# Kernel optimization log

Hardware: AMD Instinct MI355X
Metric: run time of the kernel (lower is better)

## Reference

```python
import jax, jax.numpy as jnp
import numpy as np

N_NODES = 100000
N_EDGES = 1600000
IN_C = 16
OUT_C = 16
N_EATTR = 8


def setup_inputs() -> dict:
    key = jax.random.key(0)
    k1, k2, k3, k4 = jax.random.split(key, 4)
    x = jax.random.normal(k1, (N_NODES, IN_C), dtype=jnp.float32)
    edge_index = jax.random.randint(k2, (2, N_EDGES), 0, N_NODES, dtype=jnp.int64)
    edge_attr = jax.random.normal(k3, (N_EDGES, N_EATTR), dtype=jnp.float32)
    # learned params (original inits to ones/zeros; use small random for a non-degenerate baseline)
    weight_matrix = jax.random.normal(k4, (N_EATTR, OUT_C, IN_C), dtype=jnp.float32) * 0.1
    bias = jnp.zeros((OUT_C,), dtype=jnp.float32)
    return {
        "x": x,
        "edge_index": edge_index,
        "edge_attr": edge_attr,
        "weight_matrix": weight_matrix,
        "bias": bias,
        "num_nodes": N_NODES,
    }


def reference(x, edge_index, edge_attr, weight_matrix, bias, num_nodes):
    # message: per-edge weight W_e = edge_attr @ weight_matrix (-> [E, out, in]),
    # then msg_e = W_e @ x[src_e]. Fused in one einsum to avoid the [E,out,in] blow-up.
    src = edge_index[0]
    dst = edge_index[1]
    x_j = x[src]                                   # [E, in]
    msg = jnp.einsum('ea,aoi,ei->eo', edge_attr, weight_matrix, x_j)  # [E, out]
    # aggregate: scatter-add messages to destination nodes
    aggr = jax.ops.segment_sum(msg, dst, num_segments=num_nodes)      # [N, out]
    # update: bias + relu
    return jax.nn.relu(aggr + bias)
```

## Files before the change

### kernel.cpp

```cpp
#include <hip/hip_runtime.h>


#define IN_C 16
#define OUT_C 16
#define NA 8

typedef unsigned short u16;

__device__ __forceinline__ float bfbits(unsigned hi) {
    union { unsigned u; float f; } c; c.u = hi; return c.f;
}
__device__ __forceinline__ u16 f2bf(float f) {
    union { float f; unsigned u; } c; c.f = f;
    unsigned u = c.u + (0x7fffu + ((c.u >> 16) & 1u));
    return (u16)(u >> 16);
}
__device__ __forceinline__ float dot4(float4 a, float4 b) {
    float s = a.x * b.x;
    s = fmaf(a.y, b.y, s);
    s = fmaf(a.z, b.z, s);
    s = fmaf(a.w, b.w, s);
    return s;
}

__global__ void __launch_bounds__(256) k_stage1(
    const float* __restrict__ x, const float* __restrict__ W,
    const int* __restrict__ ei, long long n_edges,
    u16* __restrict__ y, float* __restrict__ out,
    int* __restrict__ flag, int n_nodes) {
    __shared__ int s_nz;
    if (blockIdx.x == 0) {
        if (threadIdx.x == 0) s_nz = 0;
        __syncthreads();
        long long lim = 2 * n_edges;
        long long step = (n_edges / 256) | 1;
        long long pos = 1 + 2 * (long long)threadIdx.x * step;
        if (pos < lim && ei[pos] != 0) atomicOr(&s_nz, 1);
        __syncthreads();
        if (threadIdx.x == 0) flag[0] = (s_nz == 0) ? 1 : 0;
    }

    __shared__ float4 Wl[OUT_C][33];
    for (int k = threadIdx.x; k < 512; k += 256) {
        int a = k >> 6, o = (k >> 2) & 15, q = k & 3;
        Wl[o][a * 4 + q] = reinterpret_cast<const float4*>(W)[k];
    }
    __syncthreads();

    int npairs = (n_nodes + 1) >> 1;
    int idx = blockIdx.x * 256 + threadIdx.x;
    if (idx >= npairs * OUT_C) return;
    int p = idx >> 4, o = idx & 15;
    int n0 = p * 2;
    bool has1 = (n0 + 1) < n_nodes;

    const float4* xp0 = reinterpret_cast<const float4*>(x + (size_t)n0 * IN_C);
    float4 X0[4] = {xp0[0], xp0[1], xp0[2], xp0[3]};
    float4 X1[4];
    if (has1) {
        const float4* xp1 = reinterpret_cast<const float4*>(x + (size_t)(n0 + 1) * IN_C);
        X1[0] = xp1[0]; X1[1] = xp1[1]; X1[2] = xp1[2]; X1[3] = xp1[3];
    }

    union { uint4 u; u16 h[8]; } pk0, pk1;
#pragma unroll
    for (int a = 0; a < NA; ++a) {
        float4 w0 = Wl[o][a * 4 + 0], w1 = Wl[o][a * 4 + 1];
        float4 w2 = Wl[o][a * 4 + 2], w3 = Wl[o][a * 4 + 3];
        float s0 = dot4(w0, X0[0]) + dot4(w1, X0[1]) + dot4(w2, X0[2]) + dot4(w3, X0[3]);
        pk0.h[a] = f2bf(s0);
        if (has1) {
            float s1 = dot4(w0, X1[0]) + dot4(w1, X1[1]) + dot4(w2, X1[2]) + dot4(w3, X1[3]);
            pk1.h[a] = f2bf(s1);
        }
    }
    reinterpret_cast<uint4*>(y + ((size_t)n0 * OUT_C + o) * NA)[0] = pk0.u;
    out[(size_t)n0 * OUT_C + o] = 0.f;
    if (has1) {
        reinterpret_cast<uint4*>(y + ((size_t)(n0 + 1) * OUT_C + o) * NA)[0] = pk1.u;
        out[(size_t)(n0 + 1) * OUT_C + o] = 0.f;
    }
}

__global__ void __launch_bounds__(256) k_stage2(
    const int* __restrict__ ei, const float* __restrict__ ea,
    const u16* __restrict__ y, float* __restrict__ out,
    const int* __restrict__ flag, long long n_edges) {
    long long idx = (long long)blockIdx.x * 256 + threadIdx.x;
    if (idx >= n_edges * OUT_C) return;
    long long e = idx >> 4;
    int o = (int)(idx & 15);
    int src, dst;
    if (flag[0]) { src = ei[2 * e]; dst = ei[2 * (n_edges + e)]; }
    else         { src = ei[e];     dst = ei[n_edges + e]; }

    const float4* ap = reinterpret_cast<const float4*>(ea + e * NA);
    float4 a0 = ap[0], a1 = ap[1];
    uint4 yu = reinterpret_cast<const uint4*>(y + ((size_t)src * OUT_C + o) * NA)[0];

    float s =      bfbits(yu.x << 16)        * a0.x;
    s = fmaf(bfbits(yu.x & 0xffff0000u), a0.y, s);
    s = fmaf(bfbits(yu.y << 16),         a0.z, s);
    s = fmaf(bfbits(yu.y & 0xffff0000u), a0.w, s);
    s = fmaf(bfbits(yu.z << 16),         a1.x, s);
    s = fmaf(bfbits(yu.z & 0xffff0000u), a1.y, s);
    s = fmaf(bfbits(yu.w << 16),         a1.z, s);
    s = fmaf(bfbits(yu.w & 0xffff0000u), a1.w, s);

    unsafeAtomicAdd(out + (size_t)dst * OUT_C + o, s);
}

__global__ void __launch_bounds__(256) k_direct(
    const float* __restrict__ x, const int* __restrict__ ei,
    const float* __restrict__ ea, const float* __restrict__ W,
    float* __restrict__ out, long long n_edges) {
    __shared__ float Wl[OUT_C][129];
    for (int k = threadIdx.x; k < NA * OUT_C * IN_C; k += 256) {
        int a = k >> 8, o = (k >> 4) & 15, i = k & 15;
        Wl[o][a * IN_C + i] = W[k];
    }
    __syncthreads();
    long long idx = (long long)blockIdx.x * 256 + threadIdx.x;
    if (idx >= n_edges * OUT_C) return;
    long long e = idx >> 4;
    int o = (int)(idx & 15);
    int src = ei[2 * e], dst = ei[2 * (n_edges + e)];
    const float4* ap = reinterpret_cast<const float4*>(ea + e * NA);
    float4 a0 = ap[0], a1 = ap[1];
    float av[NA] = {a0.x, a0.y, a0.z, a0.w, a1.x, a1.y, a1.z, a1.w};
    const float4* xp = reinterpret_cast<const float4*>(x + (size_t)src * IN_C);
    float4 x0 = xp[0], x1 = xp[1], x2 = xp[2], x3 = xp[3];
    float xv[16] = {x0.x, x0.y, x0.z, x0.w, x1.x, x1.y, x1.z, x1.w,
                    x2.x, x2.y, x2.z, x2.w, x3.x, x3.y, x3.z, x3.w};
    float s = 0.f;
#pragma unroll
    for (int a = 0; a < NA; ++a) {
        float d = 0.f;
#pragma unroll
        for (int i = 0; i < IN_C; ++i) d = fmaf(Wl[o][a * IN_C + i], xv[i], d);
        s = fmaf(av[a], d, s);
    }
    unsafeAtomicAdd(out + (size_t)dst * OUT_C + o, s);
}

__global__ void __launch_bounds__(256) k_bias_relu(
    const float* __restrict__ bias, float* __restrict__ out, int total4) {
    int idx = blockIdx.x * 256 + threadIdx.x;
    if (idx >= total4) return;
    int j0 = (idx & 3) * 4;
    const float4 b = reinterpret_cast<const float4*>(bias + j0)[0];
    float4* op = reinterpret_cast<float4*>(out) + idx;
    float4 v = op[0];
    v.x = fmaxf(v.x + b.x, 0.f);
    v.y = fmaxf(v.y + b.y, 0.f);
    v.z = fmaxf(v.z + b.z, 0.f);
    v.w = fmaxf(v.w + b.w, 0.f);
    op[0] = v;
}

extern "C" void kernel_launch(void* const* d_in, const int* in_sizes, int n_in,
                              void* d_out, int out_size, void* d_ws, size_t ws_size,
                              hipStream_t stream) {
    const float* x    = (const float*)d_in[0];
    const int*   ei   = (const int*)d_in[1];
    const float* ea   = (const float*)d_in[2];
    const float* W    = (const float*)d_in[3];
    const float* bias = (const float*)d_in[4];
    float* out = (float*)d_out;

    int n_nodes = in_sizes[0] / IN_C;
    long long n_edges = in_sizes[2] / NA;

    size_t y_bytes = (size_t)n_nodes * OUT_C * NA * sizeof(u16);
    if (ws_size >= 64 + y_bytes) {
        int* flag = (int*)d_ws;
        u16* y = (u16*)((char*)d_ws + 64);
        int npairs = (n_nodes + 1) >> 1;
        int t1 = npairs * OUT_C;
        k_stage1<<<(t1 + 255) / 256, 256, 0, stream>>>(x, W, ei, n_edges, y, out, flag, n_nodes);
        long long tE = n_edges * OUT_C;
        k_stage2<<<(int)((tE + 255) / 256), 256, 0, stream>>>(ei, ea, y, out, flag, n_edges);
    } else {
        hipMemsetAsync(d_out, 0, (size_t)n_nodes * OUT_C * sizeof(float), stream);
        long long tE = n_edges * OUT_C;
        k_direct<<<(int)((tE + 255) / 256), 256, 0, stream>>>(x, ei, ea, W, out, n_edges);
    }

    int t4 = (n_nodes * OUT_C) / 4;
    k_bias_relu<<<(t4 + 255) / 256, 256, 0, stream>>>(bias, out, t4);
}
```

Baseline: 224.5 us.

## Replace per-edge atomic scatter with CSR sort by destination and per-node gather

Builds a destination-sorted edge list each call (histogram, two-pass scan, atomic scatter of src and bf16-packed edge attributes), then aggregates per node: accumulates edge_attr-weighted x[src] into 8 partials and applies the weight matrix, bias and relu once per node. This removes the 16 float atomics per edge into the output and the separate bias/relu pass. It adds more kernel launches, per-edge atomics for counting and placement, and a serial per-node loop whose cost depends on degree balance; edge attributes are now rounded to bf16.

```diff
diff --git a/kernel.cpp b/kernel.cpp
--- a/kernel.cpp
+++ b/kernel.cpp
@@ -6,20 +6,158 @@
 #define NA 8
 
 typedef unsigned short u16;
-
-__device__ __forceinline__ float bfbits(unsigned hi) {
-    union { unsigned u; float f; } c; c.u = hi; return c.f;
+typedef unsigned int u32;
+
+__device__ __forceinline__ float bfbits(u32 hi) {
+    union { u32 u; float f; } c; c.u = hi; return c.f;
 }
 __device__ __forceinline__ u16 f2bf(float f) {
-    union { float f; unsigned u; } c; c.f = f;
-    unsigned u = c.u + (0x7fffu + ((c.u >> 16) & 1u));
+    union { float f; u32 u; } c; c.f = f;
+    u32 u = c.u + (0x7fffu + ((c.u >> 16) & 1u));
     return (u16)(u >> 16);
 }
+
+__global__ void __launch_bounds__(256) k_init(
+    const int* __restrict__ ei, long long E, int* __restrict__ flag,
+    int* __restrict__ cnt, int n_nodes) {
+    int k = blockIdx.x * 256 + threadIdx.x;
+    if (k < n_nodes) cnt[k] = 0;
+    if (blockIdx.x == 0) {
+        __shared__ int s_nz;
+        if (threadIdx.x == 0) s_nz = 0;
+        __syncthreads();
+        long long step = (E / 256) | 1;
+        long long pos = 1 + 2 * (long long)threadIdx.x * step;
+        if (pos < 2 * E && ei[pos] != 0) atomicOr(&s_nz, 1);
+        __syncthreads();
+        if (threadIdx.x == 0) flag[0] = (s_nz == 0) ? 1 : 0;
+    }
+}
+
+__global__ void __launch_bounds__(256) k_hist(
+    const int* __restrict__ ei, long long E, const int* __restrict__ flag,
+    int* __restrict__ cnt) {
+    long long e = (long long)blockIdx.x * 256 + threadIdx.x;
+    if (e >= E) return;
+    int dst = flag[0] ? ei[2 * (E + e)] : ei[E + e];
+    atomicAdd(&cnt[dst], 1);
+}
+
+__global__ void __launch_bounds__(1024) k_scan1(
+    const int* __restrict__ cnt, int n, int* __restrict__ off, int* __restrict__ aux) {
+    __shared__ int s[1024];
+    int t = threadIdx.x;
+    int gid = blockIdx.x * 1024 + t;
+    int c = (gid < n) ? cnt[gid] : 0;
+    s[t] = c;
+    __syncthreads();
+    for (int d = 1; d < 1024; d <<= 1) {
+        int v = (t >= d) ? s[t - d] : 0;
+        __syncthreads();
+        s[t] += v;
+        __syncthreads();
+    }
+    if (gid < n) off[gid] = s[t] - c;
+    if (t == 1023) aux[blockIdx.x] = s[1023];
+}
+
+__global__ void __launch_bounds__(1024) k_scan2(
+    int* __restrict__ off, int* __restrict__ cur, const int* __restrict__ aux,
+    int nblk, int n) {
+    __shared__ int s_aux[128];
+    __shared__ int s_pfx;
+    if (threadIdx.x < 128) s_aux[threadIdx.x] = (threadIdx.x < nblk) ? aux[threadIdx.x] : 0;
+    __syncthreads();
+    if (threadIdx.x == 0) {
+        int p = 0;
+        for (int j = 0; j < (int)blockIdx.x; ++j) p += s_aux[j];
+        s_pfx = p;
+    }
+    __syncthreads();
+    int gid = blockIdx.x * 1024 + threadIdx.x;
+    if (gid < n) {
+        int o = off[gid] + s_pfx;
+        off[gid] = o;
+        cur[gid] = o;
+    }
+}
+
+__global__ void __launch_bounds__(256) k_scatter(
+    const int* __restrict__ ei, const float* __restrict__ ea,
+    const int* __restrict__ flag, int* __restrict__ cur,
+    int* __restrict__ p_src, uint4* __restrict__ p_ea, long long E) {
+    long long e = (long long)blockIdx.x * 256 + threadIdx.x;
+    if (e >= E) return;
+    int src, dst;
+    if (flag[0]) { src = ei[2 * e]; dst = ei[2 * (E + e)]; }
+    else         { src = ei[e];     dst = ei[E + e]; }
+    const float4* ap = reinterpret_cast<const float4*>(ea + e * NA);
+    float4 a0 = ap[0], a1 = ap[1];
+    union { uint4 u; u16 h[8]; } pk;
+    pk.h[0] = f2bf(a0.x); pk.h[1] = f2bf(a0.y); pk.h[2] = f2bf(a0.z); pk.h[3] = f2bf(a0.w);
+    pk.h[4] = f2bf(a1.x); pk.h[5] = f2bf(a1.y); pk.h[6] = f2bf(a1.z); pk.h[7] = f2bf(a1.w);
+    int pos = atomicAdd(&cur[dst], 1);
+    p_src[pos] = src;
+    p_ea[pos] = pk.u;
+}
+
+__global__ void __launch_bounds__(256) k_aggregate(
+    const float* __restrict__ x, const float* __restrict__ W,
+    const float* __restrict__ bias,
+    const int* __restrict__ off, const int* __restrict__ cur,
+    const int* __restrict__ p_src, const uint4* __restrict__ p_ea,
+    float* __restrict__ out, int n_nodes) {
+    __shared__ float Wl[2048];
+    __shared__ float P[16 * 272];
+    for (int k = threadIdx.x; k < 2048; k += 256) Wl[k] = W[k];
+    __syncthreads();
+
+    int g = threadIdx.x >> 4;
+    int i = threadIdx.x & 15;
+    int n = blockIdx.x * 16 + g;
+
+    float T0 = 0.f, T1 = 0.f, T2 = 0.f, T3 = 0.f, T4 = 0.f, T5 = 0.f, T6 = 0.f, T7 = 0.f;
+    float bi = bias[i];
+    if (n < n_nodes) {
+        int s = off[n], e = cur[n];
+        for (int p = s; p < e; ++p) {
+            int src = p_src[p];
+            uint4 eu = p_ea[p];
+            float xv = x[(size_t)src * IN_C + i];
+            T0 = fmaf(bfbits(eu.x << 16),         xv, T0);
+            T1 = fmaf(bfbits(eu.x & 0xffff0000u), xv, T1);
+            T2 = fmaf(bfbits(eu.y << 16),         xv, T2);
+            T3 = fmaf(bfbits(eu.y & 0xffff0000u), xv, T3);
+            T4 = fmaf(bfbits(eu.z << 16),         xv, T4);
+            T5 = fmaf(bfbits(eu.z & 0xffff0000u), xv, T5);
+            T6 = fmaf(bfbits(eu.w << 16),         xv, T6);
+            T7 = fmaf(bfbits(eu.w & 0xffff0000u), xv, T7);
+        }
+    }
+    float* Pg = P + g * 272;
+#pragma unroll
+    for (int o = 0; o < 16; ++o) {
+        const float* w = Wl + o * 16 + i;
+        float pv = T0 * w[0];
+        pv = fmaf(T1, w[256],  pv);
+        pv = fmaf(T2, w[512],  pv);
+        pv = fmaf(T3, w[768],  pv);
+        pv = fmaf(T4, w[1024], pv);
+        pv = fmaf(T5, w[1280], pv);
+        pv = fmaf(T6, w[1536], pv);
+        pv = fmaf(T7, w[1792], pv);
+        Pg[i * 17 + o] = pv;
+    }
+    __syncthreads();
+    float sum = 0.f;
+#pragma unroll
+    for (int l = 0; l < 16; ++l) sum += Pg[l * 17 + i];
+    if (n < n_nodes) out[(size_t)n * OUT_C + i] = fmaxf(sum + bi, 0.f);
+}
+
 __device__ __forceinline__ float dot4(float4 a, float4 b) {
     float s = a.x * b.x;
-    s = fmaf(a.y, b.y, s);
-    s = fmaf(a.z, b.z, s);
-    s = fmaf(a.w, b.w, s);
+    s = fmaf(a.y, b.y, s); s = fmaf(a.z, b.z, s); s = fmaf(a.w, b.w, s);
     return s;
 }
 
@@ -32,28 +170,24 @@
     if (blockIdx.x == 0) {
         if (threadIdx.x == 0) s_nz = 0;
         __syncthreads();
-        long long lim = 2 * n_edges;
         long long step = (n_edges / 256) | 1;
         long long pos = 1 + 2 * (long long)threadIdx.x * step;
-        if (pos < lim && ei[pos] != 0) atomicOr(&s_nz, 1);
+        if (pos < 2 * n_edges && ei[pos] != 0) atomicOr(&s_nz, 1);
         __syncthreads();
         if (threadIdx.x == 0) flag[0] = (s_nz == 0) ? 1 : 0;
     }
-
     __shared__ float4 Wl[OUT_C][33];
     for (int k = threadIdx.x; k < 512; k += 256) {
         int a = k >> 6, o = (k >> 2) & 15, q = k & 3;
         Wl[o][a * 4 + q] = reinterpret_cast<const float4*>(W)[k];
     }
     __syncthreads();
-
     int npairs = (n_nodes + 1) >> 1;
     int idx = blockIdx.x * 256 + threadIdx.x;
     if (idx >= npairs * OUT_C) return;
     int p = idx >> 4, o = idx & 15;
     int n0 = p * 2;
     bool has1 = (n0 + 1) < n_nodes;
-
     const float4* xp0 = reinterpret_cast<const float4*>(x + (size_t)n0 * IN_C);
     float4 X0[4] = {xp0[0], xp0[1], xp0[2], xp0[3]};
     float4 X1[4];
@@ -61,7 +195,6 @@
         const float4* xp1 = reinterpret_cast<const float4*>(x + (size_t)(n0 + 1) * IN_C);
         X1[0] = xp1[0]; X1[1] = xp1[1]; X1[2] = xp1[2]; X1[3] = xp1[3];
     }
-
     union { uint4 u; u16 h[8]; } pk0, pk1;
 #pragma unroll
     for (int a = 0; a < NA; ++a) {
@@ -93,12 +226,10 @@
     int src, dst;
     if (flag[0]) { src = ei[2 * e]; dst = ei[2 * (n_edges + e)]; }
     else         { src = ei[e];     dst = ei[n_edges + e]; }
-
     const float4* ap = reinterpret_cast<const float4*>(ea + e * NA);
     float4 a0 = ap[0], a1 = ap[1];
     uint4 yu = reinterpret_cast<const uint4*>(y + ((size_t)src * OUT_C + o) * NA)[0];
-
-    float s =      bfbits(yu.x << 16)        * a0.x;
+    float s = bfbits(yu.x << 16) * a0.x;
     s = fmaf(bfbits(yu.x & 0xffff0000u), a0.y, s);
     s = fmaf(bfbits(yu.y << 16),         a0.z, s);
     s = fmaf(bfbits(yu.y & 0xffff0000u), a0.w, s);
@@ -106,8 +237,22 @@
     s = fmaf(bfbits(yu.z & 0xffff0000u), a1.y, s);
     s = fmaf(bfbits(yu.w << 16),         a1.z, s);
     s = fmaf(bfbits(yu.w & 0xffff0000u), a1.w, s);
-
     unsafeAtomicAdd(out + (size_t)dst * OUT_C + o, s);
+}
+
+__global__ void __launch_bounds__(256) k_bias_relu(
+    const float* __restrict__ bias, float* __restrict__ out, int total4) {
+    int idx = blockIdx.x * 256 + threadIdx.x;
+    if (idx >= total4) return;
+    int j0 = (idx & 3) * 4;
+    const float4 b = reinterpret_cast<const float4*>(bias + j0)[0];
+    float4* op = reinterpret_cast<float4*>(out) + idx;
+    float4 v = op[0];
+    v.x = fmaxf(v.x + b.x, 0.f);
+    v.y = fmaxf(v.y + b.y, 0.f);
+    v.z = fmaxf(v.z + b.z, 0.f);
+    v.w = fmaxf(v.w + b.w, 0.f);
+    op[0] = v;
 }
 
 __global__ void __launch_bounds__(256) k_direct(
@@ -143,20 +288,7 @@
     unsafeAtomicAdd(out + (size_t)dst * OUT_C + o, s);
 }
 
-__global__ void __launch_bounds__(256) k_bias_relu(
-    const float* __restrict__ bias, float* __restrict__ out, int total4) {
-    int idx = blockIdx.x * 256 + threadIdx.x;
-    if (idx >= total4) return;
-    int j0 = (idx & 3) * 4;
-    const float4 b = reinterpret_cast<const float4*>(bias + j0)[0];
-    float4* op = reinterpret_cast<float4*>(out) + idx;
-    float4 v = op[0];
-    v.x = fmaxf(v.x + b.x, 0.f);
-    v.y = fmaxf(v.y + b.y, 0.f);
-    v.z = fmaxf(v.z + b.z, 0.f);
-    v.w = fmaxf(v.w + b.w, 0.f);
-    op[0] = v;
-}
+static inline size_t a256(size_t v) { return (v + 255) & ~(size_t)255; }
 
 extern "C" void kernel_launch(void* const* d_in, const int* in_sizes, int n_in,
                               void* d_out, int out_size, void* d_ws, size_t ws_size,
@@ -169,23 +301,54 @@
     float* out = (float*)d_out;
 
     int n_nodes = in_sizes[0] / IN_C;
-    long long n_edges = in_sizes[2] / NA;
-
-    size_t y_bytes = (size_t)n_nodes * OUT_C * NA * sizeof(u16);
-    if (ws_size >= 64 + y_bytes) {
-        int* flag = (int*)d_ws;
-        u16* y = (u16*)((char*)d_ws + 64);
-        int npairs = (n_nodes + 1) >> 1;
-        int t1 = npairs * OUT_C;
-        k_stage1<<<(t1 + 255) / 256, 256, 0, stream>>>(x, W, ei, n_edges, y, out, flag, n_nodes);
-        long long tE = n_edges * OUT_C;
-        k_stage2<<<(int)((tE + 255) / 256), 256, 0, stream>>>(ei, ea, y, out, flag, n_edges);
+    long long E = in_sizes[2] / NA;
+
+    size_t o_flag = 0;
+    size_t o_cnt  = 256;
+    size_t o_off  = o_cnt + a256((size_t)n_nodes * 4);
+    size_t o_cur  = o_off + a256((size_t)n_nodes * 4);
+    size_t o_aux  = o_cur + a256((size_t)n_nodes * 4);
+    size_t o_psrc = o_aux + 1024;
+    size_t o_pea  = o_psrc + a256((size_t)E * 4);
+    size_t total  = o_pea + a256((size_t)E * 16);
+
+    int gE = (int)((E + 255) / 256);
+    int gN = (n_nodes + 255) / 256;
+    int nblk_scan = (n_nodes + 1023) / 1024;
+
+    if (ws_size >= total) {
+        char* w8 = (char*)d_ws;
+        int*   flag  = (int*)(w8 + o_flag);
+        int*   cnt   = (int*)(w8 + o_cnt);
+        int*   off   = (int*)(w8 + o_off);
+        int*   cur   = (int*)(w8 + o_cur);
+        int*   aux   = (int*)(w8 + o_aux);
+        int*   p_src = (int*)(w8 + o_psrc);
+        uint4* p_ea  = (uint4*)(w8 + o_pea);
+
+        k_init<<<gN, 256, 0, stream>>>(ei, E, flag, cnt, n_nodes);
+        k_hist<<<gE, 256, 0, stream>>>(ei, E, flag, cnt);
+        k_scan1<<<nblk_scan, 1024, 0, stream>>>(cnt, n_nodes, off, aux);
+        k_scan2<<<nblk_scan, 1024, 0, stream>>>(off, cur, aux, nblk_scan, n_nodes);
+        k_scatter<<<gE, 256, 0, stream>>>(ei, ea, flag, cur, p_src, p_ea, E);
+        k_aggregate<<<(n_nodes + 15) / 16, 256, 0, stream>>>(
+            x, W, bias, off, cur, p_src, p_ea, out, n_nodes);
     } else {
-        hipMemsetAsync(d_out, 0, (size_t)n_nodes * OUT_C * sizeof(float), stream);
-        long long tE = n_edges * OUT_C;
-        k_direct<<<(int)((tE + 255) / 256), 256, 0, stream>>>(x, ei, ea, W, out, n_edges);
-    }
-
-    int t4 = (n_nodes * OUT_C) / 4;
-    k_bias_relu<<<(t4 + 255) / 256, 256, 0, stream>>>(bias, out, t4);
-}
+        size_t y_bytes = (size_t)n_nodes * OUT_C * NA * sizeof(u16);
+        if (ws_size >= 64 + y_bytes) {
+            int* flag = (int*)d_ws;
+            u16* y = (u16*)((char*)d_ws + 64);
+            int npairs = (n_nodes + 1) >> 1;
+            int t1 = npairs * OUT_C;
+            k_stage1<<<(t1 + 255) / 256, 256, 0, stream>>>(x, W, ei, E, y, out, flag, n_nodes);
+            long long tE = E * OUT_C;
+            k_stage2<<<(int)((tE + 255) / 256), 256, 0, stream>>>(ei, ea, y, out, flag, E);
+        } else {
+            hipMemsetAsync(d_out, 0, (size_t)n_nodes * OUT_C * sizeof(float), stream);
+            long long tE = E * OUT_C;
+            k_direct<<<(int)((tE + 255) / 256), 256, 0, stream>>>(x, ei, ea, W, out, E);
+        }
+        int t4 = (n_nodes * OUT_C) / 4;
+        k_bias_relu<<<(t4 + 255) / 256, 256, 0, stream>>>(bias, out, t4);
+    }
+}
```

Result: slower. 345.2 us (+53.7%).

## Scatter messages with packed bf16x2 atomics into two split accumulators

Applied to the files above, without the earlier changes.

Replaces the fp32 per-output atomic scatter with a kernel where each thread computes two output channels and issues a single packed bf16x2 global atomic add. Edges alternate between two bf16 accumulation buffers by parity to spread contention, and a final kernel sums both, adds bias and applies relu. This halves the atomic count and atomic traffic but accumulates in bf16, which loses precision on high-degree nodes. It also adds a memset and a larger workspace requirement.

```diff
diff --git a/kernel.cpp b/kernel.cpp
--- a/kernel.cpp
+++ b/kernel.cpp
@@ -6,20 +6,31 @@
 #define NA 8
 
 typedef unsigned short u16;
-
-__device__ __forceinline__ float bfbits(unsigned hi) {
-    union { unsigned u; float f; } c; c.u = hi; return c.f;
+typedef unsigned int u32;
+typedef short v2s __attribute__((ext_vector_type(2)));
+
+__device__ __forceinline__ float bfbits(u32 hi) {
+    union { u32 u; float f; } c; c.u = hi; return c.f;
 }
 __device__ __forceinline__ u16 f2bf(float f) {
-    union { float f; unsigned u; } c; c.f = f;
-    unsigned u = c.u + (0x7fffu + ((c.u >> 16) & 1u));
+    union { float f; u32 u; } c; c.f = f;
+    u32 u = c.u + (0x7fffu + ((c.u >> 16) & 1u));
     return (u16)(u >> 16);
 }
 __device__ __forceinline__ float dot4(float4 a, float4 b) {
     float s = a.x * b.x;
-    s = fmaf(a.y, b.y, s);
-    s = fmaf(a.z, b.z, s);
-    s = fmaf(a.w, b.w, s);
+    s = fmaf(a.y, b.y, s); s = fmaf(a.z, b.z, s); s = fmaf(a.w, b.w, s);
+    return s;
+}
+__device__ __forceinline__ float dot8y(uint4 yu, float4 a0, float4 a1) {
+    float s = bfbits(yu.x << 16) * a0.x;
+    s = fmaf(bfbits(yu.x & 0xffff0000u), a0.y, s);
+    s = fmaf(bfbits(yu.y << 16),         a0.z, s);
+    s = fmaf(bfbits(yu.y & 0xffff0000u), a0.w, s);
+    s = fmaf(bfbits(yu.z << 16),         a1.x, s);
+    s = fmaf(bfbits(yu.z & 0xffff0000u), a1.y, s);
+    s = fmaf(bfbits(yu.w << 16),         a1.z, s);
+    s = fmaf(bfbits(yu.w & 0xffff0000u), a1.w, s);
     return s;
 }
 
@@ -32,28 +43,24 @@
     if (blockIdx.x == 0) {
         if (threadIdx.x == 0) s_nz = 0;
         __syncthreads();
-        long long lim = 2 * n_edges;
         long long step = (n_edges / 256) | 1;
         long long pos = 1 + 2 * (long long)threadIdx.x * step;
-        if (pos < lim && ei[pos] != 0) atomicOr(&s_nz, 1);
+        if (pos < 2 * n_edges && ei[pos] != 0) atomicOr(&s_nz, 1);
         __syncthreads();
         if (threadIdx.x == 0) flag[0] = (s_nz == 0) ? 1 : 0;
     }
-
     __shared__ float4 Wl[OUT_C][33];
     for (int k = threadIdx.x; k < 512; k += 256) {
         int a = k >> 6, o = (k >> 2) & 15, q = k & 3;
         Wl[o][a * 4 + q] = reinterpret_cast<const float4*>(W)[k];
     }
     __syncthreads();
-
     int npairs = (n_nodes + 1) >> 1;
     int idx = blockIdx.x * 256 + threadIdx.x;
     if (idx >= npairs * OUT_C) return;
     int p = idx >> 4, o = idx & 15;
     int n0 = p * 2;
     bool has1 = (n0 + 1) < n_nodes;
-
     const float4* xp0 = reinterpret_cast<const float4*>(x + (size_t)n0 * IN_C);
     float4 X0[4] = {xp0[0], xp0[1], xp0[2], xp0[3]};
     float4 X1[4];
@@ -61,7 +68,6 @@
         const float4* xp1 = reinterpret_cast<const float4*>(x + (size_t)(n0 + 1) * IN_C);
         X1[0] = xp1[0]; X1[1] = xp1[1]; X1[2] = xp1[2]; X1[3] = xp1[3];
     }
-
     union { uint4 u; u16 h[8]; } pk0, pk1;
 #pragma unroll
     for (int a = 0; a < NA; ++a) {
@@ -80,6 +86,67 @@
         reinterpret_cast<uint4*>(y + ((size_t)(n0 + 1) * OUT_C + o) * NA)[0] = pk1.u;
         out[(size_t)(n0 + 1) * OUT_C + o] = 0.f;
     }
+}
+
+__global__ void __launch_bounds__(256) k_stage2_pk(
+    const int* __restrict__ ei, const float* __restrict__ ea,
+    const u16* __restrict__ y, u16* __restrict__ bufA, u16* __restrict__ bufB,
+    const int* __restrict__ flag, long long n_edges) {
+    long long gid = (long long)blockIdx.x * 256 + threadIdx.x;
+    if (gid >= n_edges * 8) return;
+    long long e = gid >> 3;
+    int q = (int)(gid & 7);
+    int src, dst;
+    if (flag[0]) { src = ei[2 * e]; dst = ei[2 * (n_edges + e)]; }
+    else         { src = ei[e];     dst = ei[n_edges + e]; }
+
+    const float4* ap = reinterpret_cast<const float4*>(ea + e * NA);
+    float4 a0 = ap[0], a1 = ap[1];
+
+    const uint4* yp = reinterpret_cast<const uint4*>(y + ((size_t)src * OUT_C + 2 * q) * NA);
+    float s0 = dot8y(yp[0], a0, a1);
+    float s1 = dot8y(yp[1], a0, a1);
+
+    union { v2s v; u16 h[2]; } pk;
+    pk.h[0] = f2bf(s0);
+    pk.h[1] = f2bf(s1);
+    u16* target = (e & 1) ? bufB : bufA;
+    v2s* addr = reinterpret_cast<v2s*>(target + (size_t)dst * OUT_C + 2 * q);
+    __builtin_amdgcn_global_atomic_fadd_v2bf16(addr, pk.v);
+}
+
+__global__ void __launch_bounds__(256) k_final_pk(
+    const u16* __restrict__ bufA, const u16* __restrict__ bufB,
+    const float* __restrict__ bias, float* __restrict__ out, int total8) {
+    int idx = blockIdx.x * 256 + threadIdx.x;
+    if (idx >= total8) return;
+    uint4 ua = reinterpret_cast<const uint4*>(bufA)[idx];
+    uint4 ub = reinterpret_cast<const uint4*>(bufB)[idx];
+    int ob = (idx & 1) * 8;
+    const float4 b0 = reinterpret_cast<const float4*>(bias + ob)[0];
+    const float4 b1 = reinterpret_cast<const float4*>(bias + ob + 4)[0];
+    float fa[8], fb[8];
+    u32 au[4] = {ua.x, ua.y, ua.z, ua.w}, bu[4] = {ub.x, ub.y, ub.z, ub.w};
+#pragma unroll
+    for (int j = 0; j < 4; ++j) {
+        fa[2 * j]     = bfbits(au[j] << 16);
+        fa[2 * j + 1] = bfbits(au[j] & 0xffff0000u);
+        fb[2 * j]     = bfbits(bu[j] << 16);
+        fb[2 * j + 1] = bfbits(bu[j] & 0xffff0000u);
+    }
+    float bb[8] = {b0.x, b0.y, b0.z, b0.w, b1.x, b1.y, b1.z, b1.w};
+    float4 o0, o1;
+    o0.x = fmaxf(fa[0] + fb[0] + bb[0], 0.f);
+    o0.y = fmaxf(fa[1] + fb[1] + bb[1], 0.f);
+    o0.z = fmaxf(fa[2] + fb[2] + bb[2], 0.f);
+    o0.w = fmaxf(fa[3] + fb[3] + bb[3], 0.f);
+    o1.x = fmaxf(fa[4] + fb[4] + bb[4], 0.f);
+    o1.y = fmaxf(fa[5] + fb[5] + bb[5], 0.f);
+    o1.z = fmaxf(fa[6] + fb[6] + bb[6], 0.f);
+    o1.w = fmaxf(fa[7] + fb[7] + bb[7], 0.f);
+    float4* op = reinterpret_cast<float4*>(out) + (size_t)idx * 2;
+    op[0] = o0;
+    op[1] = o1;
 }
 
 __global__ void __launch_bounds__(256) k_stage2(
@@ -93,21 +160,26 @@
     int src, dst;
     if (flag[0]) { src = ei[2 * e]; dst = ei[2 * (n_edges + e)]; }
     else         { src = ei[e];     dst = ei[n_edges + e]; }
-
     const float4* ap = reinterpret_cast<const float4*>(ea + e * NA);
     float4 a0 = ap[0], a1 = ap[1];
     uint4 yu = reinterpret_cast<const uint4*>(y + ((size_t)src * OUT_C + o) * NA)[0];
-
-    float s =      bfbits(yu.x << 16)        * a0.x;
-    s = fmaf(bfbits(yu.x & 0xffff0000u), a0.y, s);
-    s = fmaf(bfbits(yu.y << 16),         a0.z, s);
-    s = fmaf(bfbits(yu.y & 0xffff0000u), a0.w, s);
-    s = fmaf(bfbits(yu.z << 16),         a1.x, s);
-    s = fmaf(bfbits(yu.z & 0xffff0000u), a1.y, s);
-    s = fmaf(bfbits(yu.w << 16),         a1.z, s);
-    s = fmaf(bfbits(yu.w & 0xffff0000u), a1.w, s);
-
+    float s = dot8y(yu, a0, a1);
     unsafeAtomicAdd(out + (size_t)dst * OUT_C + o, s);
+}
+
+__global__ void __launch_bounds__(256) k_bias_relu(
+    const float* __restrict__ bias, float* __restrict__ out, int total4) {
+    int idx = blockIdx.x * 256 + threadIdx.x;
+    if (idx >= total4) return;
+    int j0 = (idx & 3) * 4;
+    const float4 b = reinterpret_cast<const float4*>(bias + j0)[0];
+    float4* op = reinterpret_cast<float4*>(out) + idx;
+    float4 v = op[0];
+    v.x = fmaxf(v.x + b.x, 0.f);
+    v.y = fmaxf(v.y + b.y, 0.f);
+    v.z = fmaxf(v.z + b.z, 0.f);
+    v.w = fmaxf(v.w + b.w, 0.f);
+    op[0] = v;
 }
 
 __global__ void __launch_bounds__(256) k_direct(
@@ -143,20 +215,7 @@
     unsafeAtomicAdd(out + (size_t)dst * OUT_C + o, s);
 }
 
-__global__ void __launch_bounds__(256) k_bias_relu(
-    const float* __restrict__ bias, float* __restrict__ out, int total4) {
-    int idx = blockIdx.x * 256 + threadIdx.x;
-    if (idx >= total4) return;
-    int j0 = (idx & 3) * 4;
-    const float4 b = reinterpret_cast<const float4*>(bias + j0)[0];
-    float4* op = reinterpret_cast<float4*>(out) + idx;
-    float4 v = op[0];
-    v.x = fmaxf(v.x + b.x, 0.f);
-    v.y = fmaxf(v.y + b.y, 0.f);
-    v.z = fmaxf(v.z + b.z, 0.f);
-    v.w = fmaxf(v.w + b.w, 0.f);
-    op[0] = v;
-}
+static inline size_t a256(size_t v) { return (v + 255) & ~(size_t)255; }
 
 extern "C" void kernel_launch(void* const* d_in, const int* in_sizes, int n_in,
                               void* d_out, int out_size, void* d_ws, size_t ws_size,
@@ -169,23 +228,43 @@
     float* out = (float*)d_out;
 
     int n_nodes = in_sizes[0] / IN_C;
-    long long n_edges = in_sizes[2] / NA;
-
+    long long E = in_sizes[2] / NA;
+
+    size_t o_flag = 0;
+    size_t o_y    = 256;
     size_t y_bytes = (size_t)n_nodes * OUT_C * NA * sizeof(u16);
-    if (ws_size >= 64 + y_bytes) {
+    size_t o_bufA = o_y + a256(y_bytes);
+    size_t buf_bytes = (size_t)n_nodes * OUT_C * sizeof(u16);
+    size_t o_bufB = o_bufA + a256(buf_bytes);
+    size_t total_pk = o_bufB + a256(buf_bytes);
+
+    int npairs = (n_nodes + 1) >> 1;
+    int g1 = (npairs * OUT_C + 255) / 256;
+
+    if (ws_size >= total_pk) {
         int* flag = (int*)d_ws;
-        u16* y = (u16*)((char*)d_ws + 64);
-        int npairs = (n_nodes + 1) >> 1;
-        int t1 = npairs * OUT_C;
-        k_stage1<<<(t1 + 255) / 256, 256, 0, stream>>>(x, W, ei, n_edges, y, out, flag, n_nodes);
-        long long tE = n_edges * OUT_C;
-        k_stage2<<<(int)((tE + 255) / 256), 256, 0, stream>>>(ei, ea, y, out, flag, n_edges);
+        u16* y    = (u16*)((char*)d_ws + o_y);
+        u16* bufA = (u16*)((char*)d_ws + o_bufA);
+        u16* bufB = (u16*)((char*)d_ws + o_bufB);
+        hipMemsetAsync((char*)d_ws + o_bufA, 0, a256(buf_bytes) + a256(buf_bytes), stream);
+        k_stage1<<<g1, 256, 0, stream>>>(x, W, ei, E, y, out, flag, n_nodes);
+        long long t2 = E * 8;
+        k_stage2_pk<<<(int)((t2 + 255) / 256), 256, 0, stream>>>(ei, ea, y, bufA, bufB, flag, E);
+        int t3 = (n_nodes * OUT_C) / 8;
+        k_final_pk<<<(t3 + 255) / 256, 256, 0, stream>>>(bufA, bufB, bias, out, t3);
+    } else if (ws_size >= 256 + y_bytes) {
+        int* flag = (int*)d_ws;
+        u16* y    = (u16*)((char*)d_ws + o_y);
+        k_stage1<<<g1, 256, 0, stream>>>(x, W, ei, E, y, out, flag, n_nodes);
+        long long tE = E * OUT_C;
+        k_stage2<<<(int)((tE + 255) / 256), 256, 0, stream>>>(ei, ea, y, out, flag, E);
+        int t4 = (n_nodes * OUT_C) / 4;
+        k_bias_relu<<<(t4 + 255) / 256, 256, 0, stream>>>(bias, out, t4);
     } else {
         hipMemsetAsync(d_out, 0, (size_t)n_nodes * OUT_C * sizeof(float), stream);
-        long long tE = n_edges * OUT_C;
-        k_direct<<<(int)((tE + 255) / 256), 256, 0, stream>>>(x, ei, ea, W, out, n_edges);
-    }
-
-    int t4 = (n_nodes * OUT_C) / 4;
-    k_bias_relu<<<(t4 + 255) / 256, 256, 0, stream>>>(bias, out, t4);
-}
+        long long tE = E * OUT_C;
+        k_direct<<<(int)((tE + 255) / 256), 256, 0, stream>>>(x, ei, ea, W, out, E);
+        int t4 = (n_nodes * OUT_C) / 4;
+        k_bias_relu<<<(t4 + 255) / 256, 256, 0, stream>>>(bias, out, t4);
+    }
+}
```

Result: faster. 200.1 us (-10.9%).
